# Kernel tuning notes

Measured on AMD Instinct MI355X. Metric: run time of the kernel, lower is better.

## Reference

```python
import jax, jax.numpy as jnp
import numpy as np

N, C, H, T, V, W, L, F = 98304, 256, 8, 64, 48, 2048, 2, 1024
DH = C // H
SCALE = 1.0 / np.sqrt(DH)


def _layer_norm(x, s, b):
    m = jnp.mean(x, axis=-1, keepdims=True)
    var = jnp.mean((x - m) ** 2, axis=-1, keepdims=True)
    return (x - m) * jax.lax.rsqrt(var + 1e-5) * s + b


def setup_inputs() -> dict:
    key = jax.random.key(0)
    ks = jax.random.split(key, 8)
    feat = jax.random.normal(ks[0], (N, C), jnp.float32)
    pos_embed = jax.random.normal(ks[1], (L, W, T, C), jnp.float32) * 0.1
    # each attention has its own (shifted) voxel->window assignment: a permutation
    # of the N voxels into W windows of V valid tokens, padded to T with dummy id N
    idx_list = []
    for l in range(L):
        perm = jax.random.permutation(jax.random.fold_in(ks[2], l), N).reshape(W, V)
        pad = jnp.full((W, T - V), N, dtype=perm.dtype)
        idx_list.append(jnp.concatenate([perm, pad], axis=1))
    win_inds = jnp.stack(idx_list).astype(jnp.int32)          # [L, W, T]
    padding_mask = jnp.broadcast_to(jnp.arange(T) >= V, (L, W, T))  # True = pad
    s = 0.02
    in_proj_w = jax.random.normal(ks[3], (L, 3 * C, C), jnp.float32) * s
    in_proj_b = jnp.zeros((L, 3 * C), jnp.float32)
    out_proj_w = jax.random.normal(ks[4], (L, C, C), jnp.float32) * s
    out_proj_b = jnp.zeros((L, C), jnp.float32)
    lin1_w = jax.random.normal(ks[5], (L, F, C), jnp.float32) * s
    lin1_b = jnp.zeros((L, F), jnp.float32)
    lin2_w = jax.random.normal(ks[6], (L, C, F), jnp.float32) * s
    lin2_b = jnp.zeros((L, C), jnp.float32)
    return dict(feat=feat, pos_embed=pos_embed, win_inds=win_inds, padding_mask=padding_mask,
                in_proj_w=in_proj_w, in_proj_b=in_proj_b, out_proj_w=out_proj_w, out_proj_b=out_proj_b,
                lin1_w=lin1_w, lin1_b=lin1_b, lin2_w=lin2_w, lin2_b=lin2_b,
                ln1_s=jnp.ones((L, C), jnp.float32), ln1_b=jnp.zeros((L, C), jnp.float32),
                ln2_s=jnp.ones((L, C), jnp.float32), ln2_b=jnp.zeros((L, C), jnp.float32))


def _sst_layer(feat, pos, mask, idx, ipw, ipb, opw, opb, l1w, l1b, l2w, l2b, n1s, n1b, n2s, n2b):
    # seq_to_win: gather voxels into windows [W, T, C]; pad slots gather voxel 0 but are masked
    gidx = jnp.where(mask, 0, idx)
    x = feat[gidx]
    qk = x + pos                                    # q = k = feat + pos, v = feat
    wq, wk, wv = jnp.split(ipw, 3, axis=0)
    bq, bk, bv = jnp.split(ipb, 3, axis=0)
    q = (qk @ wq.T + bq).reshape(W, T, H, DH)
    k = (qk @ wk.T + bk).reshape(W, T, H, DH)
    v = (x @ wv.T + bv).reshape(W, T, H, DH)
    scores = jnp.einsum('wthd,wshd->whts', q, k) * SCALE
    scores = jnp.where(mask[:, None, None, :], -1e9, scores)  # key_padding_mask
    attn = jax.nn.softmax(scores, axis=-1)
    o = jnp.einsum('whts,wshd->wthd', attn, v).reshape(W, T, C)
    o = o @ opw.T + opb
    # win_to_seq: scatter valid tokens back; pads go to dummy slot N and are dropped
    attn_seq = jnp.zeros((N + 1, C), feat.dtype).at[idx.reshape(-1)].set(o.reshape(-1, C))[:N]
    feat = _layer_norm(feat + attn_seq, n1s, n1b)   # post-norm
    ffn = jax.nn.gelu(feat @ l1w.T + l1b, approximate=False) @ l2w.T + l2b
    return _layer_norm(feat + ffn, n2s, n2b)


def reference(feat, pos_embed, win_inds, padding_mask, in_proj_w, in_proj_b, out_proj_w, out_proj_b,
              lin1_w, lin1_b, lin2_w, lin2_b, ln1_s, ln1_b, ln2_s, ln2_b):
    for l in range(L):
        feat = _sst_layer(feat, pos_embed[l], padding_mask[l], win_inds[l],
                          in_proj_w[l], in_proj_b[l], out_proj_w[l], out_proj_b[l],
                          lin1_w[l], lin1_b[l], lin2_w[l], lin2_b[l],
                          ln1_s[l], ln1_b[l], ln2_s[l], ln2_b[l])
    return feat
```

## Files before the change

kernel.cpp:

```cpp
#include <hip/hip_runtime.h>
#include <math.h>

#define N_VOX 98304
#define C_DIM 256
#define H_NUM 8
#define T_WIN 64
#define V_VAL 48
#define W_NUM 2048
#define F_DIM 1024
#define D_HEAD 32

typedef __attribute__((ext_vector_type(8))) short bf16x8;
typedef __attribute__((ext_vector_type(4))) float f32x4;
typedef __attribute__((ext_vector_type(8))) unsigned short u16x8;

__device__ __forceinline__ float4 ld4(const float* p) {
    return *reinterpret_cast<const float4*>(p);
}

__device__ __forceinline__ int swz(int f) { return f ^ ((f >> 3) & 7); }

__device__ __forceinline__ void split8(const float4& x, const float4& y, u16x8& h, u16x8& l) {
    float v[8] = {x.x, x.y, x.z, x.w, y.x, y.y, y.z, y.w};
#pragma unroll
    for (int e = 0; e < 8; e++) {
        unsigned int u = __float_as_uint(v[e]);
        h[e] = (unsigned short)(u >> 16);
        float r = v[e] - __uint_as_float(u & 0xFFFF0000u);
        l[e] = (unsigned short)(__float_as_uint(r) >> 16);
    }
}

__global__ __launch_bounds__(256)
void conv_weights(const float* __restrict__ ipw, const float* __restrict__ opw,
                  const float* __restrict__ l1w, const float* __restrict__ l2w,
                  unsigned short* __restrict__ whi, unsigned short* __restrict__ wlo)
{
    for (int c = blockIdx.x * 256 + threadIdx.x; c < 196608; c += gridDim.x * 256) {
        const int e = c * 8;
        const float* src; int base, K;
        if      (e <  196608) { src = ipw;          base = 0;       K = 256;  }
        else if (e <  393216) { src = ipw + 196608; base = 196608;  K = 256;  }
        else if (e <  458752) { src = opw;          base = 393216;  K = 256;  }
        else if (e <  524288) { src = opw + 65536;  base = 458752;  K = 256;  }
        else if (e <  786432) { src = l1w;          base = 524288;  K = 256;  }
        else if (e < 1048576) { src = l1w + 262144; base = 786432;  K = 256;  }
        else if (e < 1310720) { src = l2w;          base = 1048576; K = 1024; }
        else                  { src = l2w + 262144; base = 1310720; K = 1024; }
        const int cc = c - (base >> 3);
        const int lane = cc & 63;
        const int fk = cc >> 6;
        const int KB = K >> 5;
        const int kb = fk % KB;
        const int nb = fk / KB;
        const int srow = nb * 16 + (lane & 15);
        const int scol = kb * 32 + (lane >> 4) * 8;
        float4 x = ld4(src + (size_t)srow * K + scol);
        float4 y = ld4(src + (size_t)srow * K + scol + 4);
        u16x8 h, l;
        split8(x, y, h, l);
        *reinterpret_cast<u16x8*>(whi + e) = h;
        *reinterpret_cast<u16x8*>(wlo + e) = l;
    }
}

template<int MODE>
__global__ __launch_bounds__(512)
void gemm_mfma(const float* __restrict__ A, const float* __restrict__ feat,
               const int* __restrict__ winds, const float* __restrict__ pos,
               const unsigned short* __restrict__ Whi, const unsigned short* __restrict__ Wlo,
               const float* __restrict__ bias,
               float* __restrict__ out0, float* __restrict__ out1, float* __restrict__ out2,
               int Nc, int K)
{
    __shared__ unsigned short sAh[512 * 8];
    __shared__ unsigned short sAl[512 * 8];
    const int tid = threadIdx.x;
    const int m0 = blockIdx.x * 128;
    const int n0 = blockIdx.y * 256;
    const int KB = K >> 5;

    float* outp = out0;
    bool addpos = false;
    if (MODE == 1) {
        int grp = blockIdx.y;
        outp = (grp == 0) ? out0 : (grp == 1 ? out1 : out2);
        addpos = (grp < 2);
    }

    const int sr = tid >> 2;
    const int sq = tid & 3;
    size_t ga, gp = 0;
    const float* Asrc;
    if (MODE == 1) {
        int r = m0 + sr;
        int w = r / V_VAL, v = r - w * V_VAL;
        int t = w * T_WIN + v;
        ga = (size_t)winds[t] * C_DIM;
        gp = (size_t)t * C_DIM;
        Asrc = feat;
    } else {
        ga = (size_t)(m0 + sr) * K;
        Asrc = A;
    }

    const int wid = tid >> 6, lane = tid & 63;
    const int wm = wid & 1, wn = wid >> 1;
    const int lr = lane & 15, lg = lane >> 4;

    f32x4 acc[4][4];
#pragma unroll
    for (int i = 0; i < 4; i++)
#pragma unroll
        for (int j = 0; j < 4; j++) acc[i][j] = (f32x4){0.f, 0.f, 0.f, 0.f};

    float4 a0 = ld4(Asrc + ga + sq * 8);
    float4 a1 = ld4(Asrc + ga + sq * 8 + 4);
    if (MODE == 1 && addpos) {
        float4 p0 = ld4(pos + gp + sq * 8);
        float4 p1 = ld4(pos + gp + sq * 8 + 4);
        a0.x += p0.x; a0.y += p0.y; a0.z += p0.z; a0.w += p0.w;
        a1.x += p1.x; a1.y += p1.y; a1.z += p1.z; a1.w += p1.w;
    }

    for (int k0 = 0; k0 < K; k0 += 32) {
        u16x8 h0, l0;
        split8(a0, a1, h0, l0);
        const int f0 = sr * 4 + sq;
        __syncthreads();
        *reinterpret_cast<u16x8*>(sAh + swz(f0) * 8) = h0;
        *reinterpret_cast<u16x8*>(sAl + swz(f0) * 8) = l0;
        __syncthreads();

        if (k0 + 32 < K) {
            const float* ap = Asrc + ga + k0 + 32 + sq * 8;
            a0 = ld4(ap); a1 = ld4(ap + 4);
            if (MODE == 1 && addpos) {
                const float* pp = pos + gp + k0 + 32 + sq * 8;
                float4 p0 = ld4(pp), p1 = ld4(pp + 4);
                a0.x += p0.x; a0.y += p0.y; a0.z += p0.z; a0.w += p0.w;
                a1.x += p1.x; a1.y += p1.y; a1.z += p1.z; a1.w += p1.w;
            }
        }

        bf16x8 a_h[4], a_l[4];
#pragma unroll
        for (int i = 0; i < 4; i++) {
            int f = (wm * 64 + i * 16 + lr) * 4 + lg;
            int o = swz(f) * 8;
            a_h[i] = *reinterpret_cast<const bf16x8*>(sAh + o);
            a_l[i] = *reinterpret_cast<const bf16x8*>(sAl + o);
        }

        const int kb = k0 >> 5;
#pragma unroll
        for (int j = 0; j < 4; j++) {
            const int nb = (n0 + wn * 64 + j * 16) >> 4;
            const size_t boff = ((size_t)(nb * KB + kb) * 64 + lane) * 8;
            bf16x8 b_h = *reinterpret_cast<const bf16x8*>(Whi + boff);
            bf16x8 b_l = *reinterpret_cast<const bf16x8*>(Wlo + boff);
#pragma unroll
            for (int i = 0; i < 4; i++) {
                acc[i][j] = __builtin_amdgcn_mfma_f32_16x16x32_bf16(a_h[i], b_l, acc[i][j], 0, 0, 0);
                acc[i][j] = __builtin_amdgcn_mfma_f32_16x16x32_bf16(a_l[i], b_h, acc[i][j], 0, 0, 0);
                acc[i][j] = __builtin_amdgcn_mfma_f32_16x16x32_bf16(a_h[i], b_h, acc[i][j], 0, 0, 0);
            }
        }
    }

    float bj[4];
#pragma unroll
    for (int j = 0; j < 4; j++) bj[j] = bias[n0 + wn * 64 + j * 16 + lr];
    const int cbase = ((MODE == 1) ? 0 : n0) + wn * 64 + lr;

#pragma unroll
    for (int i = 0; i < 4; i++) {
        size_t rbase[4];
#pragma unroll
        for (int rg = 0; rg < 4; rg++) {
            int rr = m0 + wm * 64 + i * 16 + lg * 4 + rg;
            if (MODE == 2) {
                int w = rr / V_VAL, vv = rr - w * V_VAL;
                rbase[rg] = (size_t)winds[w * T_WIN + vv] * C_DIM;
            } else if (MODE == 1) {
                rbase[rg] = (size_t)rr * C_DIM;
            } else {
                rbase[rg] = (size_t)rr * (size_t)Nc;
            }
        }
#pragma unroll
        for (int j = 0; j < 4; j++) {
#pragma unroll
            for (int rg = 0; rg < 4; rg++) {
                float t = acc[i][j][rg] + bj[j];
                if (MODE == 3) t = 0.5f * t * (1.f + erff(t * 0.70710678118654752f));
                outp[rbase[rg] + cbase + j * 16] = t;
            }
        }
    }
}

__global__ __launch_bounds__(256)
void attn_win(float* __restrict__ q, const float* __restrict__ k, const float* __restrict__ v)
{
    __shared__ float qs[V_VAL][D_HEAD + 1];
    __shared__ float ks[V_VAL][D_HEAD + 1];
    __shared__ float vs[V_VAL][D_HEAD + 1];
    __shared__ float ss[V_VAL][V_VAL + 1];
    const int tid = threadIdx.x;
    const int wid = blockIdx.x >> 3;
    const int h = blockIdx.x & 7;
    const size_t base = (size_t)(wid * V_VAL) * C_DIM + h * D_HEAD;

    for (int e = tid; e < V_VAL * D_HEAD; e += 256) {
        int t = e >> 5, d = e & 31;
        size_t src = base + (size_t)t * C_DIM + d;
        qs[t][d] = q[src];
        ks[t][d] = k[src];
        vs[t][d] = v[src];
    }
    __syncthreads();

    const int si = (tid >> 4) * 3, sj = (tid & 15) * 3;
    float a00=0,a01=0,a02=0,a10=0,a11=0,a12=0,a20=0,a21=0,a22=0;
#pragma unroll
    for (int kk = 0; kk < D_HEAD; kk++) {
        float q0 = qs[si][kk], q1 = qs[si+1][kk], q2 = qs[si+2][kk];
        float k0 = ks[sj][kk], k1 = ks[sj+1][kk], k2 = ks[sj+2][kk];
        a00 += q0*k0; a01 += q0*k1; a02 += q0*k2;
        a10 += q1*k0; a11 += q1*k1; a12 += q1*k2;
        a20 += q2*k0; a21 += q2*k1; a22 += q2*k2;
    }
    const float scale = 0.17677669529663687f;
    ss[si  ][sj] = a00*scale; ss[si  ][sj+1] = a01*scale; ss[si  ][sj+2] = a02*scale;
    ss[si+1][sj] = a10*scale; ss[si+1][sj+1] = a11*scale; ss[si+1][sj+2] = a12*scale;
    ss[si+2][sj] = a20*scale; ss[si+2][sj+1] = a21*scale; ss[si+2][sj+2] = a22*scale;
    __syncthreads();

    if (tid < V_VAL) {
        float m = -1e30f;
        for (int j = 0; j < V_VAL; j++) m = fmaxf(m, ss[tid][j]);
        float sum = 0.f;
        for (int j = 0; j < V_VAL; j++) {
            float e = expf(ss[tid][j] - m);
            ss[tid][j] = e;
            sum += e;
        }
        float inv = 1.f / sum;
        for (int j = 0; j < V_VAL; j++) ss[tid][j] *= inv;
    }
    __syncthreads();

    const int oi = (tid >> 4) * 3, oj = (tid & 15) * 2;
    float o00=0,o01=0,o10=0,o11=0,o20=0,o21=0;
#pragma unroll 4
    for (int t = 0; t < V_VAL; t++) {
        float p0 = ss[oi][t], p1 = ss[oi+1][t], p2 = ss[oi+2][t];
        float v0 = vs[t][oj], v1 = vs[t][oj+1];
        o00 += p0*v0; o01 += p0*v1;
        o10 += p1*v0; o11 += p1*v1;
        o20 += p2*v0; o21 += p2*v1;
    }
    q[base + (size_t)(oi  ) * C_DIM + oj] = o00; q[base + (size_t)(oi  ) * C_DIM + oj + 1] = o01;
    q[base + (size_t)(oi+1) * C_DIM + oj] = o10; q[base + (size_t)(oi+1) * C_DIM + oj + 1] = o11;
    q[base + (size_t)(oi+2) * C_DIM + oj] = o20; q[base + (size_t)(oi+2) * C_DIM + oj + 1] = o21;
}

__global__ __launch_bounds__(256)
void ln_res(const float* __restrict__ x, const float* __restrict__ r,
            const float* __restrict__ s, const float* __restrict__ b,
            float* __restrict__ out)
{
    const int row = blockIdx.x * 4 + (threadIdx.x >> 6);
    const int lane = threadIdx.x & 63;
    const size_t off = (size_t)row * C_DIM + lane * 4;
    float4 xv = ld4(x + off);
    float4 rv = ld4(r + off);
    float tx = xv.x + rv.x, ty = xv.y + rv.y, tz = xv.z + rv.z, tw = xv.w + rv.w;
    float sum = tx + ty + tz + tw;
#pragma unroll
    for (int m = 32; m >= 1; m >>= 1) sum += __shfl_xor(sum, m, 64);
    const float mean = sum * (1.0f / 256.0f);
    float dx = tx - mean, dy = ty - mean, dz = tz - mean, dw = tw - mean;
    float sq = dx*dx + dy*dy + dz*dz + dw*dw;
#pragma unroll
    for (int m = 32; m >= 1; m >>= 1) sq += __shfl_xor(sq, m, 64);
    const float inv = rsqrtf(sq * (1.0f / 256.0f) + 1e-5f);
    const int c = lane * 4;
    float4 sv = ld4(s + c);
    float4 bv = ld4(b + c);
    float4 o;
    o.x = dx * inv * sv.x + bv.x;
    o.y = dy * inv * sv.y + bv.y;
    o.z = dz * inv * sv.z + bv.z;
    o.w = dw * inv * sv.w + bv.w;
    *reinterpret_cast<float4*>(out + off) = o;
}

extern "C" void kernel_launch(void* const* d_in, const int* in_sizes, int n_in,
                              void* d_out, int out_size, void* d_ws, size_t ws_size,
                              hipStream_t stream)
{
    const float* feat_in = (const float*)d_in[0];
    const float* pos     = (const float*)d_in[1];
    const int*   winds   = (const int*)d_in[2];
    const float* ipw = (const float*)d_in[4];
    const float* ipb = (const float*)d_in[5];
    const float* opw = (const float*)d_in[6];
    const float* opb = (const float*)d_in[7];
    const float* l1w = (const float*)d_in[8];
    const float* l1b = (const float*)d_in[9];
    const float* l2w = (const float*)d_in[10];
    const float* l2b = (const float*)d_in[11];
    const float* n1s = (const float*)d_in[12];
    const float* n1b = (const float*)d_in[13];
    const float* n2s = (const float*)d_in[14];
    const float* n2b = (const float*)d_in[15];

    float* feat_out = (float*)d_out;
    float* ws = (float*)d_ws;

    const size_t nc = (size_t)N_VOX * C_DIM;
    float* q    = ws;
    float* kbuf = ws + nc;
    float* vbuf = ws + 2 * nc;
    float* aseq = kbuf;
    float* mid  = ws;
    float* tmp  = ws + 2 * nc;

    unsigned short* whi = (unsigned short*)(ws + 3 * nc);
    unsigned short* wlo = whi + 1572864;

    const dim3 blk256(256);
    const dim3 blk512(512);
    const int NH = N_VOX / 2;

    conv_weights<<<dim3(768), blk256, 0, stream>>>(ipw, opw, l1w, l2w, whi, wlo);

    for (int l = 0; l < 2; l++) {
        const float* fin = (l == 0) ? feat_in : feat_out;
        const int*   wl  = winds + (size_t)l * W_NUM * T_WIN;
        const float* pl  = pos + (size_t)l * W_NUM * T_WIN * C_DIM;

        const unsigned short* ipw_h = whi + (size_t)l * 196608;
        const unsigned short* ipw_l = wlo + (size_t)l * 196608;
        const unsigned short* opw_h = whi + 393216 + (size_t)l * 65536;
        const unsigned short* opw_l = wlo + 393216 + (size_t)l * 65536;
        const unsigned short* l1w_h = whi + 524288 + (size_t)l * 262144;
        const unsigned short* l1w_l = wlo + 524288 + (size_t)l * 262144;
        const unsigned short* l2w_h = whi + 1048576 + (size_t)l * 262144;
        const unsigned short* l2w_l = wlo + 1048576 + (size_t)l * 262144;

        gemm_mfma<1><<<dim3(768, 3), blk512, 0, stream>>>(
            nullptr, fin, wl, pl, ipw_h, ipw_l,
            ipb + (size_t)l * 3 * C_DIM, q, kbuf, vbuf, 3 * C_DIM, C_DIM);

        attn_win<<<dim3(W_NUM * H_NUM), blk256, 0, stream>>>(q, kbuf, vbuf);

        gemm_mfma<2><<<dim3(768, 1), blk512, 0, stream>>>(
            q, nullptr, wl, nullptr, opw_h, opw_l,
            opb + (size_t)l * C_DIM, aseq, nullptr, nullptr, C_DIM, C_DIM);

        ln_res<<<dim3(N_VOX / 4), blk256, 0, stream>>>(
            fin, aseq, n1s + (size_t)l * C_DIM, n1b + (size_t)l * C_DIM, feat_out);

        for (int c = 0; c < 2; c++) {
            const float* fchunk = feat_out + (size_t)c * NH * C_DIM;
            gemm_mfma<3><<<dim3(NH / 128, F_DIM / 256), blk512, 0, stream>>>(
                fchunk, nullptr, nullptr, nullptr, l1w_h, l1w_l,
                l1b + (size_t)l * F_DIM, mid, nullptr, nullptr, F_DIM, C_DIM);
            gemm_mfma<0><<<dim3(NH / 128, 1), blk512, 0, stream>>>(
                mid, nullptr, nullptr, nullptr, l2w_h, l2w_l,
                l2b + (size_t)l * C_DIM, tmp, nullptr, nullptr, C_DIM, F_DIM);
            ln_res<<<dim3(NH / 4), blk256, 0, stream>>>(
                fchunk, tmp, n2s + (size_t)l * C_DIM, n2b + (size_t)l * C_DIM,
                feat_out + (size_t)c * NH * C_DIM);
        }
    }
}
```

Before: 3.412 ms.

## Double-buffer A tile in LDS and shrink GEMM blocks to 128x128 with 256 threads

The split-bf16 MFMA GEMM now uses 256-thread blocks covering a 128x128 output tile instead of 512 threads covering 128x256, with launch bounds requesting three blocks per CU. The A tile in shared memory is double-buffered, so the next k-slice is split and stored after the MFMAs and only one barrier is needed per iteration. B fragments are loaded into registers before the A reads. The goal is to cut barrier stalls and overlap global loads with compute, at the cost of twice as many blocks and more register pressure per thread.

Result: faster. 2.736 ms (-19.8%).

```diff
diff --git a/kernel.cpp b/kernel.cpp
--- a/kernel.cpp
+++ b/kernel.cpp
@@ -65,7 +65,7 @@
 }
 
 template<int MODE>
-__global__ __launch_bounds__(512)
+__global__ __launch_bounds__(256, 3)
 void gemm_mfma(const float* __restrict__ A, const float* __restrict__ feat,
                const int* __restrict__ winds, const float* __restrict__ pos,
                const unsigned short* __restrict__ Whi, const unsigned short* __restrict__ Wlo,
@@ -73,23 +73,25 @@
                float* __restrict__ out0, float* __restrict__ out1, float* __restrict__ out2,
                int Nc, int K)
 {
-    __shared__ unsigned short sAh[512 * 8];
-    __shared__ unsigned short sAl[512 * 8];
+    __shared__ unsigned short sAh[2][512 * 8];
+    __shared__ unsigned short sAl[2][512 * 8];
     const int tid = threadIdx.x;
     const int m0 = blockIdx.x * 128;
-    const int n0 = blockIdx.y * 256;
+    const int n0 = blockIdx.y * 128;
     const int KB = K >> 5;
 
     float* outp = out0;
+    int ncol = n0;
     bool addpos = false;
     if (MODE == 1) {
-        int grp = blockIdx.y;
+        int grp = n0 >> 8;
         outp = (grp == 0) ? out0 : (grp == 1 ? out1 : out2);
+        ncol = n0 & 255;
         addpos = (grp < 2);
     }
 
-    const int sr = tid >> 2;
-    const int sq = tid & 3;
+    const int sr = tid >> 1;
+    const int sh = tid & 1;
     size_t ga, gp = 0;
     const float* Asrc;
     if (MODE == 1) {
@@ -114,33 +116,55 @@
 #pragma unroll
         for (int j = 0; j < 4; j++) acc[i][j] = (f32x4){0.f, 0.f, 0.f, 0.f};
 
-    float4 a0 = ld4(Asrc + ga + sq * 8);
-    float4 a1 = ld4(Asrc + ga + sq * 8 + 4);
-    if (MODE == 1 && addpos) {
-        float4 p0 = ld4(pos + gp + sq * 8);
-        float4 p1 = ld4(pos + gp + sq * 8 + 4);
-        a0.x += p0.x; a0.y += p0.y; a0.z += p0.z; a0.w += p0.w;
-        a1.x += p1.x; a1.y += p1.y; a1.z += p1.z; a1.w += p1.w;
-    }
-
+    float4 a0, a1, a2, a3;
+    {
+        const float* ap = Asrc + ga + sh * 16;
+        a0 = ld4(ap); a1 = ld4(ap + 4); a2 = ld4(ap + 8); a3 = ld4(ap + 12);
+        if (MODE == 1 && addpos) {
+            const float* pp = pos + gp + sh * 16;
+            float4 p0 = ld4(pp), p1 = ld4(pp + 4), p2 = ld4(pp + 8), p3 = ld4(pp + 12);
+            a0.x += p0.x; a0.y += p0.y; a0.z += p0.z; a0.w += p0.w;
+            a1.x += p1.x; a1.y += p1.y; a1.z += p1.z; a1.w += p1.w;
+            a2.x += p2.x; a2.y += p2.y; a2.z += p2.z; a2.w += p2.w;
+            a3.x += p3.x; a3.y += p3.y; a3.z += p3.z; a3.w += p3.w;
+        }
+    }
+    const int f0 = sr * 4 + sh * 2;
+    {
+        u16x8 h0, l0, h1, l1;
+        split8(a0, a1, h0, l0);
+        split8(a2, a3, h1, l1);
+        *reinterpret_cast<u16x8*>(sAh[0] + swz(f0) * 8) = h0;
+        *reinterpret_cast<u16x8*>(sAl[0] + swz(f0) * 8) = l0;
+        *reinterpret_cast<u16x8*>(sAh[0] + swz(f0 + 1) * 8) = h1;
+        *reinterpret_cast<u16x8*>(sAl[0] + swz(f0 + 1) * 8) = l1;
+    }
+    __syncthreads();
+
+    int cur = 0;
     for (int k0 = 0; k0 < K; k0 += 32) {
-        u16x8 h0, l0;
-        split8(a0, a1, h0, l0);
-        const int f0 = sr * 4 + sq;
-        __syncthreads();
-        *reinterpret_cast<u16x8*>(sAh + swz(f0) * 8) = h0;
-        *reinterpret_cast<u16x8*>(sAl + swz(f0) * 8) = l0;
-        __syncthreads();
-
-        if (k0 + 32 < K) {
-            const float* ap = Asrc + ga + k0 + 32 + sq * 8;
-            a0 = ld4(ap); a1 = ld4(ap + 4);
+        const bool more = (k0 + 32 < K);
+        if (more) {
+            const float* ap = Asrc + ga + k0 + 32 + sh * 16;
+            a0 = ld4(ap); a1 = ld4(ap + 4); a2 = ld4(ap + 8); a3 = ld4(ap + 12);
             if (MODE == 1 && addpos) {
-                const float* pp = pos + gp + k0 + 32 + sq * 8;
-                float4 p0 = ld4(pp), p1 = ld4(pp + 4);
+                const float* pp = pos + gp + k0 + 32 + sh * 16;
+                float4 p0 = ld4(pp), p1 = ld4(pp + 4), p2 = ld4(pp + 8), p3 = ld4(pp + 12);
                 a0.x += p0.x; a0.y += p0.y; a0.z += p0.z; a0.w += p0.w;
                 a1.x += p1.x; a1.y += p1.y; a1.z += p1.z; a1.w += p1.w;
+                a2.x += p2.x; a2.y += p2.y; a2.z += p2.z; a2.w += p2.w;
+                a3.x += p3.x; a3.y += p3.y; a3.z += p3.z; a3.w += p3.w;
             }
+        }
+
+        const int kb = k0 >> 5;
+        bf16x8 b_h[4], b_l[4];
+#pragma unroll
+        for (int j = 0; j < 4; j++) {
+            const int nb = (n0 + wn * 64 + j * 16) >> 4;
+            const size_t boff = ((size_t)(nb * KB + kb) * 64 + lane) * 8;
+            b_h[j] = *reinterpret_cast<const bf16x8*>(Whi + boff);
+            b_l[j] = *reinterpret_cast<const bf16x8*>(Wlo + boff);
         }
 
         bf16x8 a_h[4], a_l[4];
@@ -148,30 +172,37 @@
         for (int i = 0; i < 4; i++) {
             int f = (wm * 64 + i * 16 + lr) * 4 + lg;
             int o = swz(f) * 8;
-            a_h[i] = *reinterpret_cast<const bf16x8*>(sAh + o);
-            a_l[i] = *reinterpret_cast<const bf16x8*>(sAl + o);
-        }
-
-        const int kb = k0 >> 5;
+            a_h[i] = *reinterpret_cast<const bf16x8*>(sAh[cur] + o);
+            a_l[i] = *reinterpret_cast<const bf16x8*>(sAl[cur] + o);
+        }
+
 #pragma unroll
         for (int j = 0; j < 4; j++) {
-            const int nb = (n0 + wn * 64 + j * 16) >> 4;
-            const size_t boff = ((size_t)(nb * KB + kb) * 64 + lane) * 8;
-            bf16x8 b_h = *reinterpret_cast<const bf16x8*>(Whi + boff);
-            bf16x8 b_l = *reinterpret_cast<const bf16x8*>(Wlo + boff);
 #pragma unroll
             for (int i = 0; i < 4; i++) {
-                acc[i][j] = __builtin_amdgcn_mfma_f32_16x16x32_bf16(a_h[i], b_l, acc[i][j], 0, 0, 0);
-                acc[i][j] = __builtin_amdgcn_mfma_f32_16x16x32_bf16(a_l[i], b_h, acc[i][j], 0, 0, 0);
-                acc[i][j] = __builtin_amdgcn_mfma_f32_16x16x32_bf16(a_h[i], b_h, acc[i][j], 0, 0, 0);
+                acc[i][j] = __builtin_amdgcn_mfma_f32_16x16x32_bf16(a_h[i], b_l[j], acc[i][j], 0, 0, 0);
+                acc[i][j] = __builtin_amdgcn_mfma_f32_16x16x32_bf16(a_l[i], b_h[j], acc[i][j], 0, 0, 0);
+                acc[i][j] = __builtin_amdgcn_mfma_f32_16x16x32_bf16(a_h[i], b_h[j], acc[i][j], 0, 0, 0);
             }
         }
+
+        if (more) {
+            u16x8 h0, l0, h1, l1;
+            split8(a0, a1, h0, l0);
+            split8(a2, a3, h1, l1);
+            *reinterpret_cast<u16x8*>(sAh[cur ^ 1] + swz(f0) * 8) = h0;
+            *reinterpret_cast<u16x8*>(sAl[cur ^ 1] + swz(f0) * 8) = l0;
+            *reinterpret_cast<u16x8*>(sAh[cur ^ 1] + swz(f0 + 1) * 8) = h1;
+            *reinterpret_cast<u16x8*>(sAl[cur ^ 1] + swz(f0 + 1) * 8) = l1;
+            __syncthreads();
+            cur ^= 1;
+        }
     }
 
     float bj[4];
 #pragma unroll
     for (int j = 0; j < 4; j++) bj[j] = bias[n0 + wn * 64 + j * 16 + lr];
-    const int cbase = ((MODE == 1) ? 0 : n0) + wn * 64 + lr;
+    const int cbase = ncol + wn * 64 + lr;
 
 #pragma unroll
     for (int i = 0; i < 4; i++) {
@@ -332,7 +363,6 @@
     unsigned short* wlo = whi + 1572864;
 
     const dim3 blk256(256);
-    const dim3 blk512(512);
     const int NH = N_VOX / 2;
 
     conv_weights<<<dim3(768), blk256, 0, stream>>>(ipw, opw, l1w, l2w, whi, wlo);
@@ -351,13 +381,13 @@
         const unsigned short* l2w_h = whi + 1048576 + (size_t)l * 262144;
         const unsigned short* l2w_l = wlo + 1048576 + (size_t)l * 262144;
 
-        gemm_mfma<1><<<dim3(768, 3), blk512, 0, stream>>>(
+        gemm_mfma<1><<<dim3(768, 6), blk256, 0, stream>>>(
             nullptr, fin, wl, pl, ipw_h, ipw_l,
             ipb + (size_t)l * 3 * C_DIM, q, kbuf, vbuf, 3 * C_DIM, C_DIM);
 
         attn_win<<<dim3(W_NUM * H_NUM), blk256, 0, stream>>>(q, kbuf, vbuf);
 
-        gemm_mfma<2><<<dim3(768, 1), blk512, 0, stream>>>(
+        gemm_mfma<2><<<dim3(768, 2), blk256, 0, stream>>>(
             q, nullptr, wl, nullptr, opw_h, opw_l,
             opb + (size_t)l * C_DIM, aseq, nullptr, nullptr, C_DIM, C_DIM);
 
@@ -366,10 +396,10 @@
 
         for (int c = 0; c < 2; c++) {
             const float* fchunk = feat_out + (size_t)c * NH * C_DIM;
-            gemm_mfma<3><<<dim3(NH / 128, F_DIM / 256), blk512, 0, stream>>>(
+            gemm_mfma<3><<<dim3(NH / 128, F_DIM / 128), blk256, 0, stream>>>(
                 fchunk, nullptr, nullptr, nullptr, l1w_h, l1w_l,
                 l1b + (size_t)l * F_DIM, mid, nullptr, nullptr, F_DIM, C_DIM);
-            gemm_mfma<0><<<dim3(NH / 128, 1), blk512, 0, stream>>>(
+            gemm_mfma<0><<<dim3(NH / 128, C_DIM / 128), blk256, 0, stream>>>(
                 mid, nullptr, nullptr, nullptr, l2w_h, l2w_l,
                 l2b + (size_t)l * C_DIM, tmp, nullptr, nullptr, C_DIM, F_DIM);
             ln_res<<<dim3(NH / 4), blk256, 0, stream>>>(
```
